# Optimization experiments

Hardware: AMD Instinct MI355X
Metric: run time of the kernel (lower is better)

Reference implementation:

```python
import jax, jax.numpy as jnp
import numpy as np

HEAD_DIM = 128
N_HEADS = 32
N_KV_HEADS = 8
N_REP = N_HEADS // N_KV_HEADS


def _rope(t, cos, sin):
    # t: [b, s, h, d]; cos/sin: [s, d//2]; rotate interleaved pairs (complex mult)
    b, s, h, d = t.shape
    t = t.reshape(b, s, h, d // 2, 2)
    t0, t1 = t[..., 0], t[..., 1]
    c = cos[None, :, None, :]
    sn = sin[None, :, None, :]
    r0 = t0 * c - t1 * sn
    r1 = t0 * sn + t1 * c
    return jnp.stack([r0, r1], axis=-1).reshape(b, s, h, d)


def setup_inputs() -> dict:
    key = jax.random.key(0)
    ks = jax.random.split(key, 6)
    b, s, dim = 2, 2048, 4096
    x = jax.random.normal(ks[0], (b, s, dim), dtype=jnp.float32)
    wq = jax.random.normal(ks[1], (N_HEADS * HEAD_DIM, dim), dtype=jnp.float32) * 0.02
    wk = jax.random.normal(ks[2], (N_KV_HEADS * HEAD_DIM, dim), dtype=jnp.float32) * 0.02
    wv = jax.random.normal(ks[3], (N_KV_HEADS * HEAD_DIM, dim), dtype=jnp.float32) * 0.02
    wo = jax.random.normal(ks[4], (dim, N_HEADS * HEAD_DIM), dtype=jnp.float32) * 0.02
    # precompute_freqs_cis: theta = 10000, freqs over half head_dim
    inv = 1.0 / (10000.0 ** (np.arange(0, HEAD_DIM, 2)[: HEAD_DIM // 2] / HEAD_DIM))
    ang = np.outer(np.arange(s), inv).astype(np.float32)  # [s, d//2]
    freqs_cos = jnp.asarray(np.cos(ang))
    freqs_sin = jnp.asarray(np.sin(ang))
    # causal additive mask
    mask = jnp.triu(jnp.full((s, s), -jnp.inf, dtype=jnp.float32), k=1)
    return {"x": x, "wq": wq, "wk": wk, "wv": wv, "wo": wo,
            "freqs_cos": freqs_cos, "freqs_sin": freqs_sin, "mask": mask,
            "start_pos": 0}


def reference(x, wq, wk, wv, wo, freqs_cos, freqs_sin, mask, start_pos):
    b, s, dim = x.shape
    xq = (x @ wq.T).reshape(b, s, N_HEADS, HEAD_DIM)
    xk = (x @ wk.T).reshape(b, s, N_KV_HEADS, HEAD_DIM)
    xv = (x @ wv.T).reshape(b, s, N_KV_HEADS, HEAD_DIM)
    xq = _rope(xq, freqs_cos, freqs_sin)
    xk = _rope(xk, freqs_cos, freqs_sin)
    # full prefill (start_pos=0): keys/values == current xk/xv
    # GQA via broadcast instead of materialized repeat_kv (same math)
    q = xq.transpose(0, 2, 1, 3).reshape(b, N_KV_HEADS, N_REP, s, HEAD_DIM)
    k = xk.transpose(0, 2, 1, 3)  # [b, kvh, s, d]
    v = xv.transpose(0, 2, 1, 3)
    scores = jnp.einsum('bgnqd,bgkd->bgnqk', q, k) / jnp.sqrt(
        jnp.asarray(HEAD_DIM, dtype=x.dtype))
    scores = scores + mask[None, None, None, :, :]
    probs = jax.nn.softmax(scores.astype(jnp.float32), axis=-1).astype(x.dtype)
    out = jnp.einsum('bgnqk,bgkd->bgnqd', probs, v)  # [b, kvh, n_rep, s, d]
    out = out.reshape(b, N_HEADS, s, HEAD_DIM).transpose(0, 2, 1, 3).reshape(b, s, -1)
    return out @ wo.T
```

## Files before the change

### kernel.cpp

```cpp
#include <hip/hip_runtime.h>
#include <hip/hip_fp16.h>
#include <stdint.h>
#include <stddef.h>

typedef _Float16 f16;
typedef __attribute__((ext_vector_type(4))) _Float16 f16x4;
typedef __attribute__((ext_vector_type(8))) _Float16 f16x8;
typedef __attribute__((ext_vector_type(4))) float f32x4;
typedef __attribute__((ext_vector_type(16))) float f32x16;

__device__ __forceinline__ void gld_lds16(const void* g, void* l) {
  __builtin_amdgcn_global_load_lds((const __attribute__((address_space(1))) void*)g,
                                   (__attribute__((address_space(3))) void*)l, 16, 0, 0);
}

__device__ __forceinline__ void vm0() {
  __asm__ volatile("s_waitcnt vmcnt(0)" ::: "memory");
}

__global__ void cast_all(const float* __restrict__ x, const float* __restrict__ wq,
                         const float* __restrict__ wk, const float* __restrict__ wv,
                         const float* __restrict__ wo, f16* __restrict__ xh,
                         f16* __restrict__ wqh, f16* __restrict__ wkh,
                         f16* __restrict__ wvh, f16* __restrict__ woh) {
  int i = blockIdx.x * blockDim.x + threadIdx.x;
  const float* in;
  f16* out;
  int j = i;
  if (j < 4194304) { in = x; out = xh; }
  else if ((j -= 4194304) < 4194304) { in = wq; out = wqh; }
  else if ((j -= 4194304) < 1048576) { in = wk; out = wkh; }
  else if ((j -= 1048576) < 1048576) { in = wv; out = wvh; }
  else { j -= 1048576; in = wo; out = woh; }
  float4 v = ((const float4*)in)[j];
  f16x4 h;
  h[0] = (f16)v.x; h[1] = (f16)v.y; h[2] = (f16)v.z; h[3] = (f16)v.w;
  *(f16x4*)(out + (size_t)j * 4) = h;
}

template <int NF>
__device__ __forceinline__ void gemm_core(const f16* __restrict__ Ab,
                                          const f16* __restrict__ Bb,
                                          f16* __restrict__ lds,
                                          f32x16 acc[4][NF]) {
  constexpr int BN = NF * 128;
  constexpr int S = 16384 + BN * 64;
  constexpr int BU = BN / 64;
  const int tid = threadIdx.x, ln = tid & 63, wv = tid >> 6;
  const int wr = wv >> 2, wc = wv & 3;
  const int l31 = ln & 31, h32 = ln >> 5;
  const int x7 = l31 & 7;
#pragma unroll
  for (int mi = 0; mi < 4; ++mi)
#pragma unroll
    for (int ni = 0; ni < NF; ++ni)
#pragma unroll
      for (int r = 0; r < 16; ++r) acc[mi][ni][r] = 0.f;

  int sA[4], sB[BU];
#pragma unroll
  for (int u = 0; u < 4; ++u) {
    int P = u * 512 + tid;
    sA[u] = (P >> 3) * 4096 + (((P & 7) ^ ((P >> 3) & 7)) * 8);
  }
#pragma unroll
  for (int u = 0; u < BU; ++u) {
    int P = u * 512 + tid;
    sB[u] = (P >> 3) * 4096 + (((P & 7) ^ ((P >> 3) & 7)) * 8);
  }
  int rA[4], rB[NF];
#pragma unroll
  for (int mi = 0; mi < 4; ++mi) rA[mi] = (wr * 128 + mi * 32 + l31) * 64;
#pragma unroll
  for (int ni = 0; ni < NF; ++ni) rB[ni] = 16384 + (wc * (NF * 32) + ni * 32 + l31) * 64;

#define STAGE(BUF, K0)                                                        \
  {                                                                           \
    _Pragma("unroll") for (int u = 0; u < 4; ++u) {                           \
      gld_lds16(Ab + sA[u] + (K0), lds + (BUF) + (u * 512 + wv * 64) * 8);    \
    }                                                                         \
    _Pragma("unroll") for (int u = 0; u < BU; ++u) {                          \
      gld_lds16(Bb + sB[u] + (K0),                                            \
                lds + (BUF) + 16384 + (u * 512 + wv * 64) * 8);               \
    }                                                                         \
  }

#define TILE_COMPUTE(BUF)                                                     \
  _Pragma("unroll") for (int ks = 0; ks < 4; ++ks) {                          \
    f16x8 af[4];                                                              \
    f16x8 bf[NF];                                                             \
    int gk = ((ks * 2 + h32) ^ x7) * 8;                                       \
    _Pragma("unroll") for (int mi = 0; mi < 4; ++mi) {                        \
      af[mi] = *(const f16x8*)&lds[(BUF) + rA[mi] + gk];                      \
    }                                                                         \
    _Pragma("unroll") for (int ni = 0; ni < NF; ++ni) {                       \
      bf[ni] = *(const f16x8*)&lds[(BUF) + rB[ni] + gk];                      \
    }                                                                         \
    __builtin_amdgcn_s_setprio(1);                                            \
    _Pragma("unroll") for (int mi = 0; mi < 4; ++mi) {                        \
      _Pragma("unroll") for (int ni = 0; ni < NF; ++ni) {                     \
        acc[mi][ni] = __builtin_amdgcn_mfma_f32_32x32x16_f16(                 \
            af[mi], bf[ni], acc[mi][ni], 0, 0, 0);                            \
      }                                                                       \
    }                                                                         \
    __builtin_amdgcn_s_setprio(0);                                            \
  }

#define SYNC()                                                                \
  __builtin_amdgcn_sched_barrier(0);                                          \
  vm0();                                                                      \
  __builtin_amdgcn_s_barrier();                                               \
  __builtin_amdgcn_sched_barrier(0);

  int cur = 0, nxt = S;
  STAGE(cur, 0);
  SYNC();
#pragma unroll 1
  for (int t = 0; t < 63; ++t) {
    STAGE(nxt, (t + 1) * 64);
    TILE_COMPUTE(cur);
    SYNC();
    int tmp = cur; cur = nxt; nxt = tmp;
  }
  TILE_COMPUTE(cur);

#undef STAGE
#undef TILE_COMPUTE
#undef SYNC
}

__global__ __launch_bounds__(512, 2) void gemm_qkv(
    const f16* __restrict__ xh, const f16* __restrict__ wcat,
    f16* __restrict__ qh, f16* __restrict__ kh, f16* __restrict__ vt) {
  __shared__ __align__(16) f16 lds[81920];
  const int id = blockIdx.x;
  const int swz = (id & 7) * 32 + (id >> 3);
  const int bx = swz & 15, by = swz >> 4;
  f32x16 acc[4][3];
  gemm_core<3>(xh + (size_t)by * 256 * 4096, wcat + (size_t)bx * 384 * 4096, lds, acc);
  const int tid = threadIdx.x, ln = tid & 63, wv = tid >> 6;
  const int wr = wv >> 2, wc = wv & 3;
  const int l31 = ln & 31, h32 = ln >> 5;
#pragma unroll
  for (int mi = 0; mi < 4; ++mi)
#pragma unroll
    for (int ni = 0; ni < 3; ++ni) {
      int gc = bx * 384 + wc * 96 + ni * 32;
#pragma unroll
      for (int g = 0; g < 4; ++g) {
        int row = by * 256 + wr * 128 + mi * 32 + h32 * 4 + g * 8;
        if (gc < 4096) {
#pragma unroll
          for (int r2 = 0; r2 < 4; ++r2)
            qh[(size_t)(row + r2) * 4096 + gc + l31] = (f16)acc[mi][ni][g * 4 + r2];
        } else if (gc < 5120) {
#pragma unroll
          for (int r2 = 0; r2 < 4; ++r2)
            kh[(size_t)(row + r2) * 1024 + (gc - 4096) + l31] = (f16)acc[mi][ni][g * 4 + r2];
        } else {
          f16x4 v4;
#pragma unroll
          for (int r2 = 0; r2 < 4; ++r2) v4[r2] = (f16)acc[mi][ni][g * 4 + r2];
          int vcol = gc + l31 - 5120;
          int kv = vcol >> 7, d = vcol & 127;
          int bbv = row >> 11, sl = row & 2047;
          *(f16x4*)&vt[(((size_t)bbv * 8 + kv) * 128 + d) * 2048 + sl] = v4;
        }
      }
    }
}

__global__ void rope_qk(f16* __restrict__ qh, f16* __restrict__ kh,
                        const float* __restrict__ fc, const float* __restrict__ fs) {
  int i = blockIdx.x * blockDim.x + threadIdx.x;
  const int QG = 4096 * 32 * 16;
  f16* ptr;
  int sl, p0;
  if (i < QG) {
    int g = i & 15, head = (i >> 4) & 31, tok = i >> 9;
    sl = tok & 2047; p0 = g * 4;
    ptr = qh + (size_t)tok * 4096 + head * 128 + g * 8;
  } else {
    int j = i - QG;
    int g = j & 15, head = (j >> 4) & 7, tok = j >> 7;
    sl = tok & 2047; p0 = g * 4;
    ptr = kh + (size_t)tok * 1024 + head * 128 + g * 8;
  }
  f16x8 v = *(f16x8*)ptr;
  float4 c = *(const float4*)&fc[sl * 64 + p0];
  float4 s = *(const float4*)&fs[sl * 64 + p0];
  f16x8 o;
  o[0] = (f16)((float)v[0] * c.x - (float)v[1] * s.x);
  o[1] = (f16)((float)v[0] * s.x + (float)v[1] * c.x);
  o[2] = (f16)((float)v[2] * c.y - (float)v[3] * s.y);
  o[3] = (f16)((float)v[2] * s.y + (float)v[3] * c.y);
  o[4] = (f16)((float)v[4] * c.z - (float)v[5] * s.z);
  o[5] = (f16)((float)v[4] * s.z + (float)v[5] * c.z);
  o[6] = (f16)((float)v[6] * c.w - (float)v[7] * s.w);
  o[7] = (f16)((float)v[6] * s.w + (float)v[7] * c.w);
  *(f16x8*)ptr = o;
}

__global__ __launch_bounds__(256, 4) void attn(
    const f16* __restrict__ qh, const f16* __restrict__ kh,
    const f16* __restrict__ vt, f16* __restrict__ ao) {
  __shared__ __align__(16) f16 Kl[64 * 128];
  __shared__ __align__(16) f16 Vl[128 * 64];
  __shared__ __align__(16) f16 Pl[4][16 * 64];
  const int qt = 31 - blockIdx.x;
  const int h = blockIdx.y, bb = blockIdx.z;
  const int kvh = h >> 2;
  const int tid = threadIdx.x, ln = tid & 63, wv = tid >> 6;
  const int quad = ln >> 4, c16 = ln & 15;

  f16x8 Qf[4];
  {
    size_t qbase = ((size_t)(bb * 2048 + qt * 64 + wv * 16 + c16)) * 4096 + h * 128;
#pragma unroll
    for (int ks = 0; ks < 4; ++ks)
      Qf[ks] = *(const f16x8*)&qh[qbase + ks * 32 + quad * 8];
  }
  float m_run = -INFINITY, l_run = 0.f;
  f32x4 Ot[8];
#pragma unroll
  for (int n = 0; n < 8; ++n) { f32x4 z = {0.f, 0.f, 0.f, 0.f}; Ot[n] = z; }
  const float scale = 0.08838834764831843f;
  const int qg = qt * 64 + wv * 16 + c16;
  const int swp = ((quad ^ (c16 & 7)) * 8);
  const int swp1 = (((4 + quad) ^ (c16 & 7)) * 8);

  for (int t = 0; t <= qt; ++t) {
#pragma unroll
    for (int c = 0; c < 4; ++c) {
      int chunk = wv * 4 + c;
      int krow = chunk * 4 + (ln >> 4);
      int kg = (ln & 15) ^ (krow & 15);
      gld_lds16(&kh[((size_t)(bb * 2048 + t * 64 + krow)) * 1024 + kvh * 128 + kg * 8],
                &Kl[chunk * 512]);
    }
#pragma unroll
    for (int c = 0; c < 4; ++c) {
      int chunk = wv * 4 + c;
      int vrow = chunk * 8 + (ln >> 3);
      int vg = (ln & 7) ^ (vrow & 7);
      gld_lds16(&vt[(((size_t)bb * 8 + kvh) * 128 + vrow) * 2048 + t * 64 + vg * 8],
                &Vl[chunk * 512]);
    }
    __syncthreads();

    f32x4 Sa[4];
#pragma unroll
    for (int tn = 0; tn < 4; ++tn) {
      f32x4 z = {0.f, 0.f, 0.f, 0.f};
      Sa[tn] = z;
#pragma unroll
      for (int ks = 0; ks < 4; ++ks) {
        f16x8 kf = *(const f16x8*)&Kl[(tn * 16 + c16) * 128 + (((ks * 4 + quad) ^ c16) * 8)];
        Sa[tn] = __builtin_amdgcn_mfma_f32_16x16x32_f16(kf, Qf[ks], Sa[tn], 0, 0, 0);
      }
    }

#pragma unroll
    for (int tn = 0; tn < 4; ++tn)
#pragma unroll
      for (int r = 0; r < 4; ++r) Sa[tn][r] *= scale;
    if (t == qt) {
#pragma unroll
      for (int tn = 0; tn < 4; ++tn) {
        int kbase = t * 64 + tn * 16 + quad * 4;
#pragma unroll
        for (int r = 0; r < 4; ++r)
          if (kbase + r > qg) Sa[tn][r] = -INFINITY;
      }
    }

    float mm = -INFINITY;
#pragma unroll
    for (int tn = 0; tn < 4; ++tn)
#pragma unroll
      for (int r = 0; r < 4; ++r) mm = fmaxf(mm, Sa[tn][r]);
    mm = fmaxf(mm, __shfl_xor(mm, 16, 64));
    mm = fmaxf(mm, __shfl_xor(mm, 32, 64));
    float mn = fmaxf(m_run, mm);
    float alpha = __expf(m_run - mn);
    m_run = mn;
    float rsum = 0.f;
#pragma unroll
    for (int tn = 0; tn < 4; ++tn)
#pragma unroll
      for (int r = 0; r < 4; ++r) {
        float p = __expf(Sa[tn][r] - mn);
        Sa[tn][r] = p;
        rsum += p;
      }
    rsum += __shfl_xor(rsum, 16, 64);
    rsum += __shfl_xor(rsum, 32, 64);
    l_run = l_run * alpha + rsum;

#pragma unroll
    for (int tn = 0; tn < 4; ++tn) {
      f16x4 pk;
#pragma unroll
      for (int r = 0; r < 4; ++r) pk[r] = (f16)Sa[tn][r];
      int g = tn * 2 + (quad >> 1);
      *(f16x4*)&Pl[wv][c16 * 64 + ((g ^ (c16 & 7)) * 8) + (quad & 1) * 4] = pk;
    }

#pragma unroll
    for (int n = 0; n < 8; ++n)
#pragma unroll
      for (int r = 0; r < 4; ++r) Ot[n][r] *= alpha;

    __asm__ volatile("s_waitcnt lgkmcnt(0)" ::: "memory");

    {
      f16x8 pf0 = *(const f16x8*)&Pl[wv][c16 * 64 + swp];
      f16x8 pf1 = *(const f16x8*)&Pl[wv][c16 * 64 + swp1];
#pragma unroll
      for (int n = 0; n < 8; ++n) {
        int rowv = (n * 16 + c16) * 64;
        f16x8 vf0 = *(const f16x8*)&Vl[rowv + swp];
        Ot[n] = __builtin_amdgcn_mfma_f32_16x16x32_f16(vf0, pf0, Ot[n], 0, 0, 0);
        f16x8 vf1 = *(const f16x8*)&Vl[rowv + swp1];
        Ot[n] = __builtin_amdgcn_mfma_f32_16x16x32_f16(vf1, pf1, Ot[n], 0, 0, 0);
      }
    }
    __syncthreads();
  }

  float inv = 1.0f / l_run;
  size_t token = (size_t)(bb * 2048 + qt * 64 + wv * 16 + c16);
#pragma unroll
  for (int n = 0; n < 8; ++n) {
    f16x4 o;
#pragma unroll
    for (int r = 0; r < 4; ++r) o[r] = (f16)(Ot[n][r] * inv);
    *(f16x4*)&ao[token * 4096 + h * 128 + n * 16 + quad * 4] = o;
  }
}

__global__ __launch_bounds__(512, 2) void gemm_out(
    const f16* __restrict__ ao, const f16* __restrict__ woh, float* __restrict__ out) {
  __shared__ __align__(16) f16 lds[65536];
  const int id = blockIdx.x;
  const int swz = (id & 7) * 32 + (id >> 3);
  const int bx = swz & 15, by = swz >> 4;
  f32x16 acc[4][2];
  gemm_core<2>(ao + (size_t)by * 256 * 4096, woh + (size_t)bx * 256 * 4096, lds, acc);
  const int tid = threadIdx.x, ln = tid & 63, wv = tid >> 6;
  const int wr = wv >> 2, wc = wv & 3;
  const int l31 = ln & 31, h32 = ln >> 5;
#pragma unroll
  for (int mi = 0; mi < 4; ++mi)
#pragma unroll
    for (int ni = 0; ni < 2; ++ni) {
      int col = bx * 256 + wc * 64 + ni * 32 + l31;
#pragma unroll
      for (int g = 0; g < 4; ++g) {
        int row = by * 256 + wr * 128 + mi * 32 + h32 * 4 + g * 8;
#pragma unroll
        for (int r2 = 0; r2 < 4; ++r2)
          out[(size_t)(row + r2) * 4096 + col] = acc[mi][ni][g * 4 + r2];
      }
    }
}

extern "C" void kernel_launch(void* const* d_in, const int* in_sizes, int n_in,
                              void* d_out, int out_size, void* d_ws, size_t ws_size,
                              hipStream_t stream) {
  const float* x  = (const float*)d_in[0];
  const float* wq = (const float*)d_in[1];
  const float* wk = (const float*)d_in[2];
  const float* wv = (const float*)d_in[3];
  const float* wo = (const float*)d_in[4];
  const float* fc = (const float*)d_in[5];
  const float* fs = (const float*)d_in[6];
  float* out = (float*)d_out;

  char* ws = (char*)d_ws;
  f16* xh  = (f16*)(ws + 0);
  f16* wqh = (f16*)(ws + 33554432);
  f16* wkh = (f16*)(ws + 67108864);
  f16* wvh = (f16*)(ws + 75497472);
  f16* woh = (f16*)(ws + 83886080);
  f16* qh  = (f16*)(ws + 117440512);
  f16* kh  = (f16*)(ws + 150994944);
  f16* vt  = (f16*)(ws + 159383552);
  f16* ao  = (f16*)(ws + 167772160);

  cast_all<<<57344, 256, 0, stream>>>(x, wq, wk, wv, wo, xh, wqh, wkh, wvh, woh);
  gemm_qkv<<<256, 512, 0, stream>>>(xh, wqh, qh, kh, vt);
  rope_qk<<<10240, 256, 0, stream>>>(qh, kh, fc, fs);
  attn<<<dim3(32, 32, 2), 256, 0, stream>>>(qh, kh, vt, ao);
  gemm_out<<<256, 512, 0, stream>>>(ao, woh, out);
}
```

Before: 794.4 us.

## Prefetch K/V tiles into registers two steps ahead in attention loop

Replaces the direct global-to-LDS loads in the attention kernel with register-staged loads issued two tiles ahead. After each tile's compute, the prefetched registers are written to LDS and the next global loads are issued, so memory latency overlaps the MFMA work. It also raises wave priority around the MFMA blocks with s_setprio. This costs extra VGPRs for the staged tiles, which may pressure occupancy under launch_bounds(256,4), and adds a second barrier per iteration.

```diff
diff --git a/kernel.cpp b/kernel.cpp
--- a/kernel.cpp
+++ b/kernel.cpp
@@ -16,6 +16,9 @@
 
 __device__ __forceinline__ void vm0() {
   __asm__ volatile("s_waitcnt vmcnt(0)" ::: "memory");
+}
+__device__ __forceinline__ void lgkm0() {
+  __asm__ volatile("s_waitcnt lgkmcnt(0)" ::: "memory");
 }
 
 __global__ void cast_all(const float* __restrict__ x, const float* __restrict__ wq,
@@ -213,6 +216,35 @@
   const int tid = threadIdx.x, ln = tid & 63, wv = tid >> 6;
   const int quad = ln >> 4, c16 = ln & 15;
 
+  int kbase[4], vbase[4], ldso[4];
+#pragma unroll
+  for (int c = 0; c < 4; ++c) {
+    int chunk = wv * 4 + c;
+    int krow = chunk * 4 + (ln >> 4);
+    int kg = (ln & 15) ^ (krow & 15);
+    kbase[c] = (bb * 2048 + krow) * 1024 + kvh * 128 + kg * 8;
+    int vrow = chunk * 8 + (ln >> 3);
+    int vg = (ln & 7) ^ (vrow & 7);
+    vbase[c] = ((bb * 8 + kvh) * 128 + vrow) * 2048 + vg * 8;
+    ldso[c] = chunk * 512 + ln * 8;
+  }
+  f16x8 kreg[4], vreg[4];
+
+#define ISSUE(T)                                                              \
+  _Pragma("unroll") for (int c = 0; c < 4; ++c) {                             \
+    kreg[c] = *(const f16x8*)&kh[(size_t)kbase[c] + (T) * 65536];             \
+    vreg[c] = *(const f16x8*)&vt[(size_t)vbase[c] + (T) * 64];                \
+  }
+#define LDSW()                                                                \
+  _Pragma("unroll") for (int c = 0; c < 4; ++c) {                             \
+    *(f16x8*)&Kl[ldso[c]] = kreg[c];                                          \
+    *(f16x8*)&Vl[ldso[c]] = vreg[c];                                          \
+  }
+#define BARRIER()                                                             \
+  __builtin_amdgcn_sched_barrier(0);                                          \
+  __builtin_amdgcn_s_barrier();                                               \
+  __builtin_amdgcn_sched_barrier(0);
+
   f16x8 Qf[4];
   {
     size_t qbase = ((size_t)(bb * 2048 + qt * 64 + wv * 16 + c16)) * 4096 + h * 128;
@@ -229,35 +261,26 @@
   const int swp = ((quad ^ (c16 & 7)) * 8);
   const int swp1 = (((4 + quad) ^ (c16 & 7)) * 8);
 
+  ISSUE(0);
+  vm0();
+  LDSW();
+  if (qt > 0) ISSUE(1);
+  lgkm0();
+  BARRIER();
+
   for (int t = 0; t <= qt; ++t) {
-#pragma unroll
-    for (int c = 0; c < 4; ++c) {
-      int chunk = wv * 4 + c;
-      int krow = chunk * 4 + (ln >> 4);
-      int kg = (ln & 15) ^ (krow & 15);
-      gld_lds16(&kh[((size_t)(bb * 2048 + t * 64 + krow)) * 1024 + kvh * 128 + kg * 8],
-                &Kl[chunk * 512]);
-    }
-#pragma unroll
-    for (int c = 0; c < 4; ++c) {
-      int chunk = wv * 4 + c;
-      int vrow = chunk * 8 + (ln >> 3);
-      int vg = (ln & 7) ^ (vrow & 7);
-      gld_lds16(&vt[(((size_t)bb * 8 + kvh) * 128 + vrow) * 2048 + t * 64 + vg * 8],
-                &Vl[chunk * 512]);
-    }
-    __syncthreads();
-
     f32x4 Sa[4];
 #pragma unroll
     for (int tn = 0; tn < 4; ++tn) {
       f32x4 z = {0.f, 0.f, 0.f, 0.f};
       Sa[tn] = z;
+      __builtin_amdgcn_s_setprio(1);
 #pragma unroll
       for (int ks = 0; ks < 4; ++ks) {
         f16x8 kf = *(const f16x8*)&Kl[(tn * 16 + c16) * 128 + (((ks * 4 + quad) ^ c16) * 8)];
         Sa[tn] = __builtin_amdgcn_mfma_f32_16x16x32_f16(kf, Qf[ks], Sa[tn], 0, 0, 0);
       }
+      __builtin_amdgcn_s_setprio(0);
     }
 
 #pragma unroll
@@ -267,10 +290,10 @@
     if (t == qt) {
 #pragma unroll
       for (int tn = 0; tn < 4; ++tn) {
-        int kbase = t * 64 + tn * 16 + quad * 4;
+        int kbase2 = t * 64 + tn * 16 + quad * 4;
 #pragma unroll
         for (int r = 0; r < 4; ++r)
-          if (kbase + r > qg) Sa[tn][r] = -INFINITY;
+          if (kbase2 + r > qg) Sa[tn][r] = -INFINITY;
       }
     }
 
@@ -311,11 +334,12 @@
 #pragma unroll
       for (int r = 0; r < 4; ++r) Ot[n][r] *= alpha;
 
-    __asm__ volatile("s_waitcnt lgkmcnt(0)" ::: "memory");
+    lgkm0();
 
     {
       f16x8 pf0 = *(const f16x8*)&Pl[wv][c16 * 64 + swp];
       f16x8 pf1 = *(const f16x8*)&Pl[wv][c16 * 64 + swp1];
+      __builtin_amdgcn_s_setprio(1);
 #pragma unroll
       for (int n = 0; n < 8; ++n) {
         int rowv = (n * 16 + c16) * 64;
@@ -324,8 +348,17 @@
         f16x8 vf1 = *(const f16x8*)&Vl[rowv + swp1];
         Ot[n] = __builtin_amdgcn_mfma_f32_16x16x32_f16(vf1, pf1, Ot[n], 0, 0, 0);
       }
-    }
-    __syncthreads();
+      __builtin_amdgcn_s_setprio(0);
+    }
+
+    BARRIER();
+    if (t < qt) {
+      vm0();
+      LDSW();
+      if (t + 1 < qt) ISSUE(t + 2);
+      lgkm0();
+      BARRIER();
+    }
   }
 
   float inv = 1.0f / l_run;
@@ -337,6 +370,9 @@
     for (int r = 0; r < 4; ++r) o[r] = (f16)(Ot[n][r] * inv);
     *(f16x4*)&ao[token * 4096 + h * 128 + n * 16 + quad * 4] = o;
   }
+#undef ISSUE
+#undef LDSW
+#undef BARRIER
 }
 
 __global__ __launch_bounds__(512, 2) void gemm_out(
```

Result: slower. 1.006 ms (+26.6%).

## Load K and V fragments directly from global memory in attention

Applied to the files above, without the earlier changes.

The attention kernel no longer stages K and V tiles in shared memory with global-to-LDS loads and block barriers. Each wave now reads its MFMA K and V fragments straight from global memory, relying on the caches. This removes the LDS copies and per-tile __syncthreads. In exchange, each of the four waves fetches the same K/V data separately, and global load latency sits directly on the MFMA critical path with no prefetching.

```diff
diff --git a/kernel.cpp b/kernel.cpp
--- a/kernel.cpp
+++ b/kernel.cpp
@@ -16,6 +16,9 @@
 
 __device__ __forceinline__ void vm0() {
   __asm__ volatile("s_waitcnt vmcnt(0)" ::: "memory");
+}
+__device__ __forceinline__ void lgkm0() {
+  __asm__ volatile("s_waitcnt lgkmcnt(0)" ::: "memory");
 }
 
 __global__ void cast_all(const float* __restrict__ x, const float* __restrict__ wq,
@@ -204,8 +207,6 @@
 __global__ __launch_bounds__(256, 4) void attn(
     const f16* __restrict__ qh, const f16* __restrict__ kh,
     const f16* __restrict__ vt, f16* __restrict__ ao) {
-  __shared__ __align__(16) f16 Kl[64 * 128];
-  __shared__ __align__(16) f16 Vl[128 * 64];
   __shared__ __align__(16) f16 Pl[4][16 * 64];
   const int qt = 31 - blockIdx.x;
   const int h = blockIdx.y, bb = blockIdx.z;
@@ -229,25 +230,11 @@
   const int swp = ((quad ^ (c16 & 7)) * 8);
   const int swp1 = (((4 + quad) ^ (c16 & 7)) * 8);
 
+  const f16* kb = kh + ((size_t)(bb * 2048 + c16)) * 1024 + kvh * 128;
+  const f16* vb = vt + ((size_t)(bb * 8 + kvh) * 128 + c16) * 2048;
+
   for (int t = 0; t <= qt; ++t) {
-#pragma unroll
-    for (int c = 0; c < 4; ++c) {
-      int chunk = wv * 4 + c;
-      int krow = chunk * 4 + (ln >> 4);
-      int kg = (ln & 15) ^ (krow & 15);
-      gld_lds16(&kh[((size_t)(bb * 2048 + t * 64 + krow)) * 1024 + kvh * 128 + kg * 8],
-                &Kl[chunk * 512]);
-    }
-#pragma unroll
-    for (int c = 0; c < 4; ++c) {
-      int chunk = wv * 4 + c;
-      int vrow = chunk * 8 + (ln >> 3);
-      int vg = (ln & 7) ^ (vrow & 7);
-      gld_lds16(&vt[(((size_t)bb * 8 + kvh) * 128 + vrow) * 2048 + t * 64 + vg * 8],
-                &Vl[chunk * 512]);
-    }
-    __syncthreads();
-
+    const f16* kt = kb + (size_t)t * 64 * 1024;
     f32x4 Sa[4];
 #pragma unroll
     for (int tn = 0; tn < 4; ++tn) {
@@ -255,7 +242,7 @@
       Sa[tn] = z;
 #pragma unroll
       for (int ks = 0; ks < 4; ++ks) {
-        f16x8 kf = *(const f16x8*)&Kl[(tn * 16 + c16) * 128 + (((ks * 4 + quad) ^ c16) * 8)];
+        f16x8 kf = *(const f16x8*)&kt[(size_t)tn * 16 * 1024 + (ks * 4 + quad) * 8];
         Sa[tn] = __builtin_amdgcn_mfma_f32_16x16x32_f16(kf, Qf[ks], Sa[tn], 0, 0, 0);
       }
     }
@@ -267,10 +254,10 @@
     if (t == qt) {
 #pragma unroll
       for (int tn = 0; tn < 4; ++tn) {
-        int kbase = t * 64 + tn * 16 + quad * 4;
+        int kbase2 = t * 64 + tn * 16 + quad * 4;
 #pragma unroll
         for (int r = 0; r < 4; ++r)
-          if (kbase + r > qg) Sa[tn][r] = -INFINITY;
+          if (kbase2 + r > qg) Sa[tn][r] = -INFINITY;
       }
     }
 
@@ -311,21 +298,21 @@
 #pragma unroll
       for (int r = 0; r < 4; ++r) Ot[n][r] *= alpha;
 
-    __asm__ volatile("s_waitcnt lgkmcnt(0)" ::: "memory");
+    lgkm0();
 
     {
       f16x8 pf0 = *(const f16x8*)&Pl[wv][c16 * 64 + swp];
       f16x8 pf1 = *(const f16x8*)&Pl[wv][c16 * 64 + swp1];
+      const f16* vtl = vb + t * 64;
 #pragma unroll
       for (int n = 0; n < 8; ++n) {
-        int rowv = (n * 16 + c16) * 64;
-        f16x8 vf0 = *(const f16x8*)&Vl[rowv + swp];
+        const f16* vd = vtl + (size_t)n * 16 * 2048;
+        f16x8 vf0 = *(const f16x8*)&vd[quad * 8];
         Ot[n] = __builtin_amdgcn_mfma_f32_16x16x32_f16(vf0, pf0, Ot[n], 0, 0, 0);
-        f16x8 vf1 = *(const f16x8*)&Vl[rowv + swp1];
+        f16x8 vf1 = *(const f16x8*)&vd[32 + quad * 8];
         Ot[n] = __builtin_amdgcn_mfma_f32_16x16x32_f16(vf1, pf1, Ot[n], 0, 0, 0);
       }
     }
-    __syncthreads();
   }
 
   float inv = 1.0f / l_run;
```

After: 1.474 ms. 85.6% more time.
